# Performance work log

Hardware: AMD Instinct MI355X
Metric: run time of the kernel (lower is better)

Reference implementation:

```python
import jax, jax.numpy as jnp
import numpy as np

N, E, D, H, LAYERS = 50000, 800000, 128, 8, 2
LRELU_ALPHA = 0.2


def _seg_softmax(logits, seg, n):
    # numerically stable softmax over edges grouped by destination node
    m = jax.ops.segment_max(logits, seg, num_segments=n)
    z = jnp.exp(logits - m[seg])
    s = jax.ops.segment_sum(z, seg, num_segments=n)
    return z / jnp.maximum(s[seg], 1e-16)


def _gat_layer(x, src, dst, W, a_src, a_dst, concat):
    # W: [H, Fin, F'], a_src/a_dst: [H, F']
    n = x.shape[0]
    outs = []
    for h in range(W.shape[0]):  # loop over heads to bound peak memory
        Wh = x @ W[h]                              # [N, F']
        es = Wh @ a_src[h]                         # [N]
        ed = Wh @ a_dst[h]                         # [N]
        e = jax.nn.leaky_relu(es[src] + ed[dst], LRELU_ALPHA)  # [E]
        att = _seg_softmax(e, dst, n)              # [E]
        out = jax.ops.segment_sum(att[:, None] * Wh[src], dst, num_segments=n)
        outs.append(out)
    if concat:
        return jax.nn.elu(jnp.concatenate(outs, axis=-1))  # [N, H*F']
    return jnp.mean(jnp.stack(outs, axis=0), axis=0)        # [N, F']


def _rel_gcn_layer(x, src, dst, w, W):
    # weighted-adjacency GCN with row (in-degree) normalization + ReLU
    n = x.shape[0]
    deg = jax.ops.segment_sum(w, dst, num_segments=n)
    norm = w / jnp.maximum(deg[dst], 1e-16)        # [E]
    h = x @ W                                      # [N, Dout]
    agg = jax.ops.segment_sum(norm[:, None] * h[src], dst, num_segments=n)
    return jax.nn.relu(agg)


def setup_inputs() -> dict:
    key = jax.random.key(0)
    ks = jax.random.split(key, 12)
    s = 1.0 / np.sqrt(D)
    return {
        "x": jax.random.normal(ks[0], (N, D), dtype=jnp.float32),
        "edge_index": jax.random.randint(ks[1], (2, E), 0, N, dtype=jnp.int64),
        "edge_weight": jax.random.uniform(ks[2], (E,), dtype=jnp.float32),
        "gat_W0": jax.random.normal(ks[3], (H, D, D // H), dtype=jnp.float32) * s,
        "gat_a0_src": jax.random.normal(ks[4], (H, D // H), dtype=jnp.float32) * s,
        "gat_a0_dst": jax.random.normal(ks[5], (H, D // H), dtype=jnp.float32) * s,
        "gat_W1": jax.random.normal(ks[6], (H, D, D), dtype=jnp.float32) * s,
        "gat_a1_src": jax.random.normal(ks[7], (H, D), dtype=jnp.float32) * s,
        "gat_a1_dst": jax.random.normal(ks[8], (H, D), dtype=jnp.float32) * s,
        "gcn_W0": jax.random.normal(ks[9], (D, D), dtype=jnp.float32) * s,
        "gcn_W1": jax.random.normal(ks[10], (D, D), dtype=jnp.float32) * s,
    }


def reference(x, edge_index, edge_weight, gat_W0, gat_a0_src, gat_a0_dst,
              gat_W1, gat_a1_src, gat_a1_dst, gcn_W0, gcn_W1):
    src, dst = edge_index[0], edge_index[1]
    gat_params = [(gat_W0, gat_a0_src, gat_a0_dst), (gat_W1, gat_a1_src, gat_a1_dst)]
    gcn_params = [gcn_W0, gcn_W1]
    x1, x2 = x, x  # dropout is identity in eval mode
    for i in range(LAYERS):
        W, a_s, a_d = gat_params[i]
        x1 = _gat_layer(x1, src, dst, W, a_s, a_d, concat=(i != LAYERS - 1))
        x2 = _rel_gcn_layer(x2, src, dst, edge_weight, gcn_params[i])
    # cat along new last dim then MaxPool1d(2) == elementwise max of branches
    return jnp.maximum(x1, x2)
```

## Files before the change

### kernel.cpp

```cpp
#include <hip/hip_runtime.h>

#define LRELU_ALPHA 0.2f

typedef __attribute__((ext_vector_type(8))) short short8;
typedef __attribute__((ext_vector_type(4))) float float4v;

__device__ __forceinline__ unsigned short f2bf(float f) {
  union { float f; unsigned u; } x; x.f = f;
  unsigned r = (x.u + 0x7fff + ((x.u >> 16) & 1)) >> 16;
  return (unsigned short)r;
}
__device__ __forceinline__ float bflo(unsigned u) {
  union { unsigned u; float f; } x; x.u = u << 16; return x.f;
}
__device__ __forceinline__ float bfhi(unsigned u) {
  union { unsigned u; float f; } x; x.u = u & 0xffff0000u; return x.f;
}


__global__ __launch_bounds__(256) void k_count(const int* __restrict__ dst,
                                               int* __restrict__ cnt, int E) {
  int e = blockIdx.x * 256 + threadIdx.x;
  if (e < E) atomicAdd(&cnt[dst[e]], 1);
}

__global__ __launch_bounds__(1024) void k_scan1(const int* __restrict__ cnt,
                                                int* __restrict__ lscan,
                                                int* __restrict__ bsum, int N) {
  __shared__ int sm[1024];
  int t = threadIdx.x;
  int base = blockIdx.x * 1024;
  int v = (base + t < N) ? cnt[base + t] : 0;
  sm[t] = v;
  __syncthreads();
  for (int off = 1; off < 1024; off <<= 1) {
    int x = (t >= off) ? sm[t - off] : 0;
    __syncthreads();
    sm[t] += x;
    __syncthreads();
  }
  if (base + t < N) lscan[base + t] = sm[t] - v;
  if (t == 1023) bsum[blockIdx.x] = sm[1023];
}

__global__ __launch_bounds__(64) void k_scan2(int* __restrict__ bsum,
                                              int* __restrict__ rowptrN, int nb) {
  if (threadIdx.x == 0) {
    int run = 0;
    for (int i = 0; i < nb; ++i) {
      int v = bsum[i];
      bsum[i] = run;
      run += v;
    }
    *rowptrN = run;
  }
}

__global__ __launch_bounds__(1024) void k_scan3(int* __restrict__ rowptr,
                                                int* __restrict__ cur,
                                                const int* __restrict__ bsum, int N) {
  int i = blockIdx.x * 1024 + threadIdx.x;
  if (i < N) {
    int v = rowptr[i] + bsum[blockIdx.x];
    rowptr[i] = v;
    cur[i] = v;
  }
}

__global__ __launch_bounds__(256) void k_scatter(const int* __restrict__ src,
                                                 const int* __restrict__ dst,
                                                 const float* __restrict__ w,
                                                 int* __restrict__ cur,
                                                 uint2* __restrict__ edata, int E) {
  int e = blockIdx.x * 256 + threadIdx.x;
  if (e < E) {
    int d = dst[e];
    int p = atomicAdd(&cur[d], 1);
    edata[p] = make_uint2((unsigned)src[e], __float_as_uint(w[e]));
  }
}

__global__ __launch_bounds__(256) void k_pack(const float* __restrict__ W0,
                                              const float* __restrict__ a0s,
                                              const float* __restrict__ a0d,
                                              const float* __restrict__ W1,
                                              const float* __restrict__ a1s,
                                              const float* __restrict__ a1d,
                                              const float* __restrict__ gw0,
                                              const float* __restrict__ gw1,
                                              unsigned short* __restrict__ W0catT,
                                              float* __restrict__ logitW,
                                              unsigned short* __restrict__ gw1T,
                                              unsigned short* __restrict__ va1T,
                                              unsigned short* __restrict__ WstackT) {
  int idx = blockIdx.x * 256 + threadIdx.x;
  if (idx < 32768) {
    int n = idx >> 7, k = idx & 127;
    int q = n >> 2, r = n & 3;
    float v;
    if (r < 2) {
      int o = 2 * q + r;
      int h = o >> 4, f = o & 15;
      v = W0[h * 2048 + k * 16 + f];
    } else {
      int j = 2 * q + (r - 2);
      v = gw0[k * 128 + j];
    }
    W0catT[idx] = f2bf(v);
  } else if (idx < 34816) {
    int j = idx - 32768;
    int k = j >> 4, c = j & 15;
    int h = (c < 8) ? c : c - 8;
    const float* a = (c < 8) ? a0s : a0d;
    float s = 0.f;
    for (int f = 0; f < 16; ++f) s += W0[h * 2048 + k * 16 + f] * a[h * 16 + f];
    logitW[j] = s;
  } else if (idx < 51200) {
    int j = idx - 34816;
    int n = j >> 7, k = j & 127;
    gw1T[j] = f2bf(gw1[k * 128 + n]);
  } else if (idx < 53248) {
    int j = idx - 51200;
    int c = j >> 7, k = j & 127;
    int h = c & 7;
    const float* a = (c < 8) ? a1s : a1d;
    float s = 0.f;
    for (int f = 0; f < 128; ++f) s += W1[h * 16384 + k * 128 + f] * a[h * 128 + f];
    va1T[j] = f2bf(s);
  } else if (idx < 184320) {
    int j = idx - 53248;
    int n = j >> 10, kk = j & 1023;
    int h = kk >> 7, k = kk & 127;
    WstackT[j] = f2bf(W1[h * 16384 + k * 128 + n] * 0.125f);
  }
}

__global__ __launch_bounds__(256) void k_prep(const float* __restrict__ x,
                                              const float* __restrict__ logitW,
                                              unsigned short* __restrict__ xb,
                                              float* __restrict__ logit0, int N) {
  __shared__ float sm[16][132];
  __shared__ float sw[2048];
  int t = threadIdx.x;
  int base = blockIdx.x * 16;
  int r = t >> 4, cc = (t & 15) * 8;
  const float* xr = x + (size_t)(base + r) * 128 + cc;
  float4 v0 = *(const float4*)xr;
  float4 v1 = *(const float4*)(xr + 4);
  ushort4 o0 = {f2bf(v0.x), f2bf(v0.y), f2bf(v0.z), f2bf(v0.w)};
  ushort4 o1 = {f2bf(v1.x), f2bf(v1.y), f2bf(v1.z), f2bf(v1.w)};
  *(ushort4*)(xb + (size_t)(base + r) * 128 + cc) = o0;
  *(ushort4*)(xb + (size_t)(base + r) * 128 + cc + 4) = o1;
  *(float4*)&sm[r][cc] = v0;
  *(float4*)&sm[r][cc + 4] = v1;
  *(float4*)&sw[t * 8] = *(const float4*)(logitW + t * 8);
  *(float4*)&sw[t * 8 + 4] = *(const float4*)(logitW + t * 8 + 4);
  __syncthreads();
  int c = t & 15;
  float acc = 0.f;
#pragma unroll
  for (int k = 0; k < 128; ++k) acc += sm[r][k] * sw[k * 16 + c];
  logit0[(size_t)(base + r) * 16 + c] = acc;
}

template <int NT, int OUT_BF16, int EPI>
__global__ __launch_bounds__(256) void k_mgemm(const unsigned short* __restrict__ A, int lda,
                                               const unsigned short* __restrict__ BT, int ldb,
                                               void* __restrict__ Cv, int ldc,
                                               const float* __restrict__ aux,
                                               int M, int Ncols, int K) {
  __shared__ unsigned short As[64][64];
  __shared__ unsigned short Bs[NT * 16][64];
  int tid = threadIdx.x;
  int w = tid >> 6, lane = tid & 63;
  int quad = lane >> 4, l16 = lane & 15;
  int row0 = blockIdx.x * 64;
  int c0 = blockIdx.y * (NT * 16);
  float4v acc[NT];
#pragma unroll
  for (int t = 0; t < NT; ++t) acc[t] = (float4v){0.f, 0.f, 0.f, 0.f};

  for (int k0 = 0; k0 < K; k0 += 64) {
    __syncthreads();
#pragma unroll
    for (int i = 0; i < 2; ++i) {
      int c = tid + i * 256;
      int r = c >> 3, kc = c & 7;
      uint4 v = {0u, 0u, 0u, 0u};
      int gr = row0 + r;
      if (gr < M) v = *(const uint4*)(A + (size_t)gr * lda + k0 + kc * 8);
      *(uint4*)(&As[r][(kc ^ (r & 7)) * 8]) = v;
    }
#pragma unroll
    for (int i = 0; i < (NT * 128 + 255) / 256; ++i) {
      int c = tid + i * 256;
      if (c < NT * 128) {
        int n = c >> 3, kc = c & 7;
        uint4 v = {0u, 0u, 0u, 0u};
        int gn = c0 + n;
        if (gn < Ncols) v = *(const uint4*)(BT + (size_t)gn * ldb + k0 + kc * 8);
        *(uint4*)(&Bs[n][(kc ^ (n & 7)) * 8]) = v;
      }
    }
    __syncthreads();
#pragma unroll
    for (int ks = 0; ks < 2; ++ks) {
      int m = w * 16 + l16;
      int ga = (ks * 4 + quad) ^ (m & 7);
      short8 a = *(const short8*)(&As[m][ga * 8]);
#pragma unroll
      for (int t = 0; t < NT; ++t) {
        int n = t * 16 + l16;
        int gb = (ks * 4 + quad) ^ (n & 7);
        short8 b = *(const short8*)(&Bs[n][gb * 8]);
        acc[t] = __builtin_amdgcn_mfma_f32_16x16x32_bf16(a, b, acc[t], 0, 0, 0);
      }
    }
  }
#pragma unroll
  for (int t = 0; t < NT; ++t) {
    int cc = c0 + t * 16 + l16;
    if (cc >= Ncols) continue;
#pragma unroll
    for (int i = 0; i < 4; ++i) {
      int rr = row0 + w * 16 + quad * 4 + i;
      if (rr >= M) continue;
      float v = acc[t][i];
      if (EPI == 1) v = fmaxf(v, aux[(size_t)rr * ldc + cc]);
      if (EPI == 2) {
        ((unsigned short*)Cv)[(size_t)rr * 256 + 4 * (cc >> 1) + 2 + (cc & 1)] = f2bf(v);
      } else if (OUT_BF16)
        ((unsigned short*)Cv)[(size_t)rr * ldc + cc] = f2bf(v);
      else
        ((float*)Cv)[(size_t)rr * ldc + cc] = v;
    }
  }
}

__global__ __launch_bounds__(256) void k_agg0(const unsigned short* __restrict__ feat0i,
                                              const float* __restrict__ logit0,
                                              const int* __restrict__ rowptr,
                                              const uint2* __restrict__ edata,
                                              unsigned short* __restrict__ x1c,
                                              unsigned short* __restrict__ x2,
                                              unsigned short* __restrict__ xh, int N) {
  __shared__ uint2 swl[4][64];
  int wave = threadIdx.x >> 6, lane = threadIdx.x & 63;
  int d = blockIdx.x * 4 + wave;
  if (d >= N) return;
  int head = lane >> 3, hh = lane & 7, j8 = lane >> 3;
  float edv = logit0[(size_t)d * 16 + 8 + hh];
  int beg = rowptr[d], end = rowptr[d + 1], deg = end - beg;
  float l = 0.f, a0 = 0.f, a1 = 0.f, g0 = 0.f, g1 = 0.f, wsum = 0.f;
  for (int base = 0; base < deg; base += 64) {
    int idx = beg + base + lane;
    uint2 sv = make_uint2(0u, 0u);
    if (idx < end) sv = edata[idx];
    swl[wave][lane] = sv;
    int ng = deg - base; if (ng > 64) ng = 64;
    int groups = (ng + 7) >> 3;
    for (int g = 0; g < groups; ++g) {
      uint2 swj = swl[wave][g * 8 + j8];
      float es = logit0[(size_t)swj.x * 16 + hh];
      float lg = es + edv;
      lg = lg > 0.f ? lg : LRELU_ALPHA * lg;
      float pme = __expf(fminf(lg, 80.f));
      if (g * 8 + j8 >= ng) pme = 0.f;
#pragma unroll
      for (int j = 0; j < 8; ++j) {
        uint2 sw = swl[wave][g * 8 + j];
        float pj = __shfl(pme, j * 8 + head, 64);
        float wj = __uint_as_float(sw.y);
        uint2 u = *(const uint2*)(feat0i + (size_t)sw.x * 256 + 4 * lane);
        a0 += pj * bflo(u.x);
        a1 += pj * bfhi(u.x);
        g0 += wj * bflo(u.y);
        g1 += wj * bfhi(u.y);
        l += pj;
        wsum += wj;
      }
    }
  }
  float inv = l > 0.f ? 1.f / l : 0.f;
  float v0 = a0 * inv, v1 = a1 * inv;
  v0 = v0 > 0.f ? v0 : __expf(v0) - 1.f;
  v1 = v1 > 0.f ? v1 : __expf(v1) - 1.f;
  unsigned xpack = (unsigned)f2bf(v0) | ((unsigned)f2bf(v1) << 16);
  ((unsigned*)x1c)[(size_t)d * 64 + lane] = xpack;
  ((unsigned*)xh)[(size_t)d * 128 + 2 * lane] = xpack;
  float ginv = 1.f / fmaxf(wsum, 1e-16f);
  float w0 = fmaxf(g0 * ginv, 0.f), w1 = fmaxf(g1 * ginv, 0.f);
  ((unsigned*)x2)[(size_t)d * 64 + lane] = (unsigned)f2bf(w0) | ((unsigned)f2bf(w1) << 16);
}

__global__ __launch_bounds__(256) void k_agg1(const unsigned short* __restrict__ xh,
                                              const float* __restrict__ esed,
                                              const int* __restrict__ rowptr,
                                              const uint2* __restrict__ edata,
                                              unsigned short* __restrict__ aggbuf,
                                              float* __restrict__ x2f,
                                              int d0, int d1) {
  __shared__ uint2 swl[4][64];
  __shared__ float pl[4][64];
  int wave = threadIdx.x >> 6, lane = threadIdx.x & 63;
  int d = d0 + blockIdx.x * 4 + wave;
  if (d >= d1) return;
  int hh = lane & 7, j8 = lane >> 3;
  float ed = esed[(size_t)d * 16 + 8 + hh];
  int beg = rowptr[d], end = rowptr[d + 1], deg = end - beg;
  float ax[8] = {}, ay[8] = {};
  float lpart = 0.f, g0 = 0.f, g1 = 0.f, wsum = 0.f;
  for (int base = 0; base < deg; base += 64) {
    int idx = beg + base + lane;
    uint2 sv = make_uint2(0u, 0u);
    if (idx < end) sv = edata[idx];
    swl[wave][lane] = sv;
    int ng = deg - base; if (ng > 64) ng = 64;
    int groups = (ng + 7) >> 3;
    for (int g = 0; g < groups; ++g) {
      uint2 swj = swl[wave][g * 8 + j8];
      float es = esed[(size_t)swj.x * 16 + hh];
      float lg = es + ed;
      lg = lg > 0.f ? lg : LRELU_ALPHA * lg;
      float pme = __expf(fminf(lg, 80.f));
      if (g * 8 + j8 >= ng) pme = 0.f;
      lpart += pme;
      pl[wave][lane] = pme;
#pragma unroll
      for (int j = 0; j < 8; ++j) {
        uint2 sw = swl[wave][g * 8 + j];
        float4 pv0 = *(const float4*)&pl[wave][j * 8];
        float4 pv1 = *(const float4*)&pl[wave][j * 8 + 4];
        uint2 u = *(const uint2*)(xh + (size_t)sw.x * 256 + 4 * lane);
        float xx = bflo(u.x), xy = bfhi(u.x);
        float wj = __uint_as_float(sw.y);
        g0 += wj * bflo(u.y);
        g1 += wj * bfhi(u.y);
        wsum += wj;
        ax[0] += pv0.x * xx; ay[0] += pv0.x * xy;
        ax[1] += pv0.y * xx; ay[1] += pv0.y * xy;
        ax[2] += pv0.z * xx; ay[2] += pv0.z * xy;
        ax[3] += pv0.w * xx; ay[3] += pv0.w * xy;
        ax[4] += pv1.x * xx; ay[4] += pv1.x * xy;
        ax[5] += pv1.y * xx; ay[5] += pv1.y * xy;
        ax[6] += pv1.z * xx; ay[6] += pv1.z * xy;
        ax[7] += pv1.w * xx; ay[7] += pv1.w * xy;
      }
    }
  }
  lpart += __shfl_xor(lpart, 8, 64);
  lpart += __shfl_xor(lpart, 16, 64);
  lpart += __shfl_xor(lpart, 32, 64);
  size_t lr = (size_t)(d - d0) * 512;
#pragma unroll
  for (int h = 0; h < 8; ++h) {
    float lh = __shfl(lpart, h, 64);
    float inv = lh > 0.f ? 1.f / lh : 0.f;
    ((unsigned*)aggbuf)[lr + h * 64 + lane] =
        (unsigned)f2bf(ax[h] * inv) | ((unsigned)f2bf(ay[h] * inv) << 16);
  }
  float ginv = 1.f / fmaxf(wsum, 1e-16f);
  float w0 = fmaxf(g0 * ginv, 0.f), w1 = fmaxf(g1 * ginv, 0.f);
  *(float2*)(x2f + (size_t)d * 128 + 2 * lane) = make_float2(w0, w1);
}


extern "C" void kernel_launch(void* const* d_in, const int* in_sizes, int n_in,
                              void* d_out, int out_size, void* d_ws, size_t ws_size,
                              hipStream_t stream) {
  const float* x   = (const float*)d_in[0];
  const int*   ei  = (const int*)d_in[1];
  const float* ew  = (const float*)d_in[2];
  const float* W0  = (const float*)d_in[3];
  const float* a0s = (const float*)d_in[4];
  const float* a0d = (const float*)d_in[5];
  const float* W1  = (const float*)d_in[6];
  const float* a1s = (const float*)d_in[7];
  const float* a1d = (const float*)d_in[8];
  const float* gw0 = (const float*)d_in[9];
  const float* gw1 = (const float*)d_in[10];
  float* out = (float*)d_out;

  const int N = in_sizes[0] / 128;
  const int E = in_sizes[1] / 2;
  const int* src = ei;
  const int* dst = ei + E;

  char* p = (char*)d_ws;
  auto carve = [&](size_t bytes) {
    void* r = (void*)p;
    p += (bytes + 255) & ~(size_t)255;
    return r;
  };
  int*   cnt    = (int*)carve((size_t)N * 4);
  int*   rowptr = (int*)carve((size_t)(N + 1) * 4);
  int*   cur    = (int*)carve((size_t)N * 4);
  int*   bsum   = (int*)carve(256 * 4);
  uint2* edata  = (uint2*)carve((size_t)E * 8);
  unsigned short* W0catT  = (unsigned short*)carve(32768 * 2);
  float*          logitW  = (float*)carve(2048 * 4);
  unsigned short* gw1T    = (unsigned short*)carve(16384 * 2);
  unsigned short* va1T    = (unsigned short*)carve(2048 * 2);
  unsigned short* WstackT = (unsigned short*)carve(131072 * 2);
  unsigned short* x1c  = (unsigned short*)carve((size_t)N * 128 * 2);
  unsigned short* x2   = (unsigned short*)carve((size_t)N * 128 * 2);
  float*          x2f  = (float*)carve((size_t)N * 128 * 4);
  float*          esed = (float*)carve((size_t)N * 16 * 4);
  unsigned short* xh   = (unsigned short*)carve((size_t)N * 256 * 2);
  const int CH = 25600;
  size_t ph1 = ((size_t)N * 128 * 2 + 255) & ~(size_t)255;
  size_t ph2 = ph1 + (((size_t)N * 256 * 2 + 255) & ~(size_t)255);
  size_t ph3 = ph2 + (((size_t)N * 16 * 4 + 255) & ~(size_t)255);
  size_t scratch_sz = (size_t)CH * 1024 * 2;
  if (ph3 > scratch_sz) scratch_sz = ph3;
  char* scratch = (char*)carve(scratch_sz);
  unsigned short* xb     = (unsigned short*)scratch;
  unsigned short* feat0i = (unsigned short*)(scratch + ph1);
  float*          logit0 = (float*)(scratch + ph2);
  unsigned short* aggbuf = (unsigned short*)scratch;

  hipMemsetAsync(cnt, 0, (size_t)N * 4, stream);
  int gE = (E + 255) / 256;
  k_count<<<gE, 256, 0, stream>>>(dst, cnt, E);
  int nb = (N + 1023) / 1024;
  k_scan1<<<nb, 1024, 0, stream>>>(cnt, rowptr, bsum, N);
  k_scan2<<<1, 64, 0, stream>>>(bsum, rowptr + N, nb);
  k_scan3<<<nb, 1024, 0, stream>>>(rowptr, cur, bsum, N);
  k_scatter<<<gE, 256, 0, stream>>>(src, dst, ew, cur, edata, E);

  k_pack<<<(184320 + 255) / 256, 256, 0, stream>>>(W0, a0s, a0d, W1, a1s, a1d, gw0,
                                                   gw1, W0catT, logitW, gw1T, va1T,
                                                   WstackT);
  k_prep<<<(N + 15) / 16, 256, 0, stream>>>(x, logitW, xb, logit0, N);

  int gM = (N + 63) / 64;
  k_mgemm<8, 1, 0><<<dim3(gM, 2), 256, 0, stream>>>(xb, 128, W0catT, 128, feat0i, 256,
                                                    nullptr, N, 256, 128);
  k_agg0<<<(N + 3) / 4, 256, 0, stream>>>(feat0i, logit0, rowptr, edata,
                                          x1c, x2, xh, N);

  k_mgemm<1, 0, 0><<<dim3(gM, 1), 256, 0, stream>>>(x1c, 128, va1T, 128, esed, 16,
                                                    nullptr, N, 16, 128);
  k_mgemm<8, 1, 2><<<dim3(gM, 1), 256, 0, stream>>>(x2, 128, gw1T, 128, xh, 256,
                                                    nullptr, N, 128, 128);

  for (int d0 = 0; d0 < N; d0 += CH) {
    int d1 = d0 + CH < N ? d0 + CH : N;
    int chN = d1 - d0;
    k_agg1<<<(chN + 3) / 4, 256, 0, stream>>>(xh, esed, rowptr, edata,
                                              aggbuf, x2f, d0, d1);
    k_mgemm<8, 0, 1><<<dim3((chN + 63) / 64, 1), 256, 0, stream>>>(
        aggbuf, 1024, WstackT, 1024, out + (size_t)d0 * 128, 128,
        x2f + (size_t)d0 * 128, chN, 128, 1024);
  }
}
```

Measured before the change: 499.4 us.

## Pack aggregation accumulators as float2, store GCN branch in bf16, wave-scan block sums

Rewrites the per-edge accumulation in both aggregation kernels to use two-wide float vectors, so the compiler can emit packed FMA instructions. Stores the second-layer GCN branch output in bf16 instead of fp32, which halves its write and the read in the final max epilogue. Replaces the serial single-thread block-sum scan with a wave shuffle scan. The bf16 intermediate adds rounding error to the GCN branch before the final max. The wave scan assumes at most 64 blocks, which holds for this N.

```diff
diff --git a/kernel.cpp b/kernel.cpp
--- a/kernel.cpp
+++ b/kernel.cpp
@@ -4,6 +4,7 @@
 
 typedef __attribute__((ext_vector_type(8))) short short8;
 typedef __attribute__((ext_vector_type(4))) float float4v;
+typedef __attribute__((ext_vector_type(2))) float f32x2;
 
 __device__ __forceinline__ unsigned short f2bf(float f) {
   union { float f; unsigned u; } x; x.f = f;
@@ -15,6 +16,9 @@
 }
 __device__ __forceinline__ float bfhi(unsigned u) {
   union { unsigned u; float f; } x; x.u = u & 0xffff0000u; return x.f;
+}
+__device__ __forceinline__ f32x2 bfpair(unsigned u) {
+  return (f32x2){bflo(u), bfhi(u)};
 }
 
 
@@ -45,15 +49,15 @@
 
 __global__ __launch_bounds__(64) void k_scan2(int* __restrict__ bsum,
                                               int* __restrict__ rowptrN, int nb) {
-  if (threadIdx.x == 0) {
-    int run = 0;
-    for (int i = 0; i < nb; ++i) {
-      int v = bsum[i];
-      bsum[i] = run;
-      run += v;
-    }
-    *rowptrN = run;
-  }
+  int t = threadIdx.x;
+  int v = (t < nb) ? bsum[t] : 0;
+  int orig = v;
+  for (int off = 1; off < 64; off <<= 1) {
+    int y = __shfl_up(v, off, 64);
+    if (t >= off) v += y;
+  }
+  if (t < nb) bsum[t] = v - orig;
+  if (t == 63) *rowptrN = v;
 }
 
 __global__ __launch_bounds__(1024) void k_scan3(int* __restrict__ rowptr,
@@ -167,7 +171,7 @@
 __global__ __launch_bounds__(256) void k_mgemm(const unsigned short* __restrict__ A, int lda,
                                                const unsigned short* __restrict__ BT, int ldb,
                                                void* __restrict__ Cv, int ldc,
-                                               const float* __restrict__ aux,
+                                               const void* __restrict__ aux,
                                                int M, int Ncols, int K) {
   __shared__ unsigned short As[64][64];
   __shared__ unsigned short Bs[NT * 16][64];
@@ -226,7 +230,10 @@
       int rr = row0 + w * 16 + quad * 4 + i;
       if (rr >= M) continue;
       float v = acc[t][i];
-      if (EPI == 1) v = fmaxf(v, aux[(size_t)rr * ldc + cc]);
+      if (EPI == 1) {
+        unsigned short us = ((const unsigned short*)aux)[(size_t)rr * ldc + cc];
+        v = fmaxf(v, bflo((unsigned)us));
+      }
       if (EPI == 2) {
         ((unsigned short*)Cv)[(size_t)rr * 256 + 4 * (cc >> 1) + 2 + (cc & 1)] = f2bf(v);
       } else if (OUT_BF16)
@@ -251,7 +258,8 @@
   int head = lane >> 3, hh = lane & 7, j8 = lane >> 3;
   float edv = logit0[(size_t)d * 16 + 8 + hh];
   int beg = rowptr[d], end = rowptr[d + 1], deg = end - beg;
-  float l = 0.f, a0 = 0.f, a1 = 0.f, g0 = 0.f, g1 = 0.f, wsum = 0.f;
+  float l = 0.f, wsum = 0.f;
+  f32x2 a2 = {0.f, 0.f}, g2 = {0.f, 0.f};
   for (int base = 0; base < deg; base += 64) {
     int idx = beg + base + lane;
     uint2 sv = make_uint2(0u, 0u);
@@ -272,24 +280,22 @@
         float pj = __shfl(pme, j * 8 + head, 64);
         float wj = __uint_as_float(sw.y);
         uint2 u = *(const uint2*)(feat0i + (size_t)sw.x * 256 + 4 * lane);
-        a0 += pj * bflo(u.x);
-        a1 += pj * bfhi(u.x);
-        g0 += wj * bflo(u.y);
-        g1 += wj * bfhi(u.y);
+        a2 += bfpair(u.x) * pj;
+        g2 += bfpair(u.y) * wj;
         l += pj;
         wsum += wj;
       }
     }
   }
   float inv = l > 0.f ? 1.f / l : 0.f;
-  float v0 = a0 * inv, v1 = a1 * inv;
+  float v0 = a2.x * inv, v1 = a2.y * inv;
   v0 = v0 > 0.f ? v0 : __expf(v0) - 1.f;
   v1 = v1 > 0.f ? v1 : __expf(v1) - 1.f;
   unsigned xpack = (unsigned)f2bf(v0) | ((unsigned)f2bf(v1) << 16);
   ((unsigned*)x1c)[(size_t)d * 64 + lane] = xpack;
   ((unsigned*)xh)[(size_t)d * 128 + 2 * lane] = xpack;
   float ginv = 1.f / fmaxf(wsum, 1e-16f);
-  float w0 = fmaxf(g0 * ginv, 0.f), w1 = fmaxf(g1 * ginv, 0.f);
+  float w0 = fmaxf(g2.x * ginv, 0.f), w1 = fmaxf(g2.y * ginv, 0.f);
   ((unsigned*)x2)[(size_t)d * 64 + lane] = (unsigned)f2bf(w0) | ((unsigned)f2bf(w1) << 16);
 }
 
@@ -298,7 +304,7 @@
                                               const int* __restrict__ rowptr,
                                               const uint2* __restrict__ edata,
                                               unsigned short* __restrict__ aggbuf,
-                                              float* __restrict__ x2f,
+                                              unsigned short* __restrict__ x2f,
                                               int d0, int d1) {
   __shared__ uint2 swl[4][64];
   __shared__ float pl[4][64];
@@ -308,8 +314,9 @@
   int hh = lane & 7, j8 = lane >> 3;
   float ed = esed[(size_t)d * 16 + 8 + hh];
   int beg = rowptr[d], end = rowptr[d + 1], deg = end - beg;
-  float ax[8] = {}, ay[8] = {};
-  float lpart = 0.f, g0 = 0.f, g1 = 0.f, wsum = 0.f;
+  f32x2 ax2[8] = {};
+  f32x2 g2 = {0.f, 0.f};
+  float lpart = 0.f, wsum = 0.f;
   for (int base = 0; base < deg; base += 64) {
     int idx = beg + base + lane;
     uint2 sv = make_uint2(0u, 0u);
@@ -332,19 +339,18 @@
         float4 pv0 = *(const float4*)&pl[wave][j * 8];
         float4 pv1 = *(const float4*)&pl[wave][j * 8 + 4];
         uint2 u = *(const uint2*)(xh + (size_t)sw.x * 256 + 4 * lane);
-        float xx = bflo(u.x), xy = bfhi(u.x);
+        f32x2 xv = bfpair(u.x);
         float wj = __uint_as_float(sw.y);
-        g0 += wj * bflo(u.y);
-        g1 += wj * bfhi(u.y);
+        g2 += bfpair(u.y) * wj;
         wsum += wj;
-        ax[0] += pv0.x * xx; ay[0] += pv0.x * xy;
-        ax[1] += pv0.y * xx; ay[1] += pv0.y * xy;
-        ax[2] += pv0.z * xx; ay[2] += pv0.z * xy;
-        ax[3] += pv0.w * xx; ay[3] += pv0.w * xy;
-        ax[4] += pv1.x * xx; ay[4] += pv1.x * xy;
-        ax[5] += pv1.y * xx; ay[5] += pv1.y * xy;
-        ax[6] += pv1.z * xx; ay[6] += pv1.z * xy;
-        ax[7] += pv1.w * xx; ay[7] += pv1.w * xy;
+        ax2[0] += xv * pv0.x;
+        ax2[1] += xv * pv0.y;
+        ax2[2] += xv * pv0.z;
+        ax2[3] += xv * pv0.w;
+        ax2[4] += xv * pv1.x;
+        ax2[5] += xv * pv1.y;
+        ax2[6] += xv * pv1.z;
+        ax2[7] += xv * pv1.w;
       }
     }
   }
@@ -357,11 +363,11 @@
     float lh = __shfl(lpart, h, 64);
     float inv = lh > 0.f ? 1.f / lh : 0.f;
     ((unsigned*)aggbuf)[lr + h * 64 + lane] =
-        (unsigned)f2bf(ax[h] * inv) | ((unsigned)f2bf(ay[h] * inv) << 16);
+        (unsigned)f2bf(ax2[h].x * inv) | ((unsigned)f2bf(ax2[h].y * inv) << 16);
   }
   float ginv = 1.f / fmaxf(wsum, 1e-16f);
-  float w0 = fmaxf(g0 * ginv, 0.f), w1 = fmaxf(g1 * ginv, 0.f);
-  *(float2*)(x2f + (size_t)d * 128 + 2 * lane) = make_float2(w0, w1);
+  float w0 = fmaxf(g2.x * ginv, 0.f), w1 = fmaxf(g2.y * ginv, 0.f);
+  ((unsigned*)x2f)[(size_t)d * 64 + lane] = (unsigned)f2bf(w0) | ((unsigned)f2bf(w1) << 16);
 }
 
 
@@ -404,7 +410,7 @@
   unsigned short* WstackT = (unsigned short*)carve(131072 * 2);
   unsigned short* x1c  = (unsigned short*)carve((size_t)N * 128 * 2);
   unsigned short* x2   = (unsigned short*)carve((size_t)N * 128 * 2);
-  float*          x2f  = (float*)carve((size_t)N * 128 * 4);
+  unsigned short* x2f  = (unsigned short*)carve((size_t)N * 128 * 2);
   float*          esed = (float*)carve((size_t)N * 16 * 4);
   unsigned short* xh   = (unsigned short*)carve((size_t)N * 256 * 2);
   const int CH = 25600;
```

Result: faster. 488.0 us (-2.3%).
